# Kernel tuning notes

Hardware: AMD Instinct MI355X
Metric: run time of the kernel (lower is better)

The kernel has to match this reference:

```python
import jax, jax.numpy as jnp
import numpy as np

N, E, IN, H, D = 50000, 800000, 256, 4, 32
NEG_SLOPE = 0.2


def setup_inputs() -> dict:
    key = jax.random.key(0)
    ks = jax.random.split(key, 11)
    feat = jax.random.normal(ks[0], (N, IN), jnp.float32)
    src = jax.random.randint(ks[1], (E,), 0, N, jnp.int32)
    dst = jax.random.randint(ks[2], (E,), 0, N, jnp.int32)
    # ppmi in [1, 10) so log(log(ppmi)) path is non-trivial
    ppmi = 1.0 + 9.0 * jax.random.uniform(ks[3], (E,), jnp.float32)
    eps_src = jax.random.normal(ks[4], (N, H, 1), jnp.float32)
    eps_dst = jax.random.normal(ks[5], (N, H, 1), jnp.float32)
    W = jax.random.normal(ks[6], (IN, H * D), jnp.float32) * (1.0 / np.sqrt(IN))
    mu_src = jax.random.normal(ks[7], (1, H, D), jnp.float32) * 0.02
    mu_dst = jax.random.normal(ks[8], (1, H, D), jnp.float32) * 0.02
    lam_src = jax.random.normal(ks[9], (1, H, D), jnp.float32) * 0.02
    lam_dst = jax.random.normal(ks[10], (1, H, D), jnp.float32) * 0.02
    return dict(feat=feat, src=src, dst=dst, ppmi=ppmi, eps_src=eps_src,
                eps_dst=eps_dst, W=W, mu_src=mu_src, mu_dst=mu_dst,
                lam_src=lam_src, lam_dst=lam_dst)


def reference(feat, src, dst, ppmi, eps_src, eps_dst, W, mu_src, mu_dst, lam_src, lam_dst):
    n = feat.shape[0]
    h, d = mu_src.shape[1], mu_src.shape[2]
    ft = (feat @ W).reshape(n, h, d)                      # [N,H,D]
    # per-node attention scalars (src == dst node set here)
    mu_s = (ft * mu_src).sum(-1, keepdims=True)           # [N,H,1]
    lam_s = (ft * lam_src).sum(-1, keepdims=True)
    mu_d = (ft * mu_dst).sum(-1, keepdims=True)
    lam_d = (ft * lam_src).sum(-1, keepdims=True)         # original uses lam_src here (replicated)
    # reparameterize z = eps * exp(0.5*logvar) + mu
    z_src = eps_src * jnp.exp(0.5 * lam_s) + mu_s
    z_dst = eps_dst * jnp.exp(0.5 * lam_d) + mu_d
    e = jax.nn.leaky_relu(z_src[src] + z_dst[dst], NEG_SLOPE)   # [E,H,1]
    scale = jnp.clip(jnp.log(jnp.clip(jnp.log(ppmi), 1.0, None)), 1.0, None)
    e2 = e * scale[:, None, None]
    # edge softmax over destination segments
    emax = jax.ops.segment_max(e2, dst, num_segments=n)   # [N,H,1]
    ee = jnp.exp(e2 - emax[dst])
    denom = jax.ops.segment_sum(ee, dst, num_segments=n)
    a = ee / denom[dst]                                    # [E,H,1]
    # weighted scatter-sum aggregation: u_mul_e + sum
    rst = jax.ops.segment_sum(ft[src] * a, dst, num_segments=n)  # [N,H,D]
    return rst, mu_s + mu_d, lam_s + lam_d
```

## Files before the change

### kernel.cpp

```cpp
#include <hip/hip_runtime.h>

#define N_NODES 50000
#define N_EDGES 800000
#define IN_DIM  256
#define NH      4
#define HD      128
#define NEG_SLOPE 0.2f
#define SCAN_BLOCKS ((N_NODES + 255) / 256)

typedef short          v8s __attribute__((ext_vector_type(8)));
typedef float          v4f __attribute__((ext_vector_type(4)));
typedef unsigned short us8 __attribute__((ext_vector_type(8)));

__device__ __forceinline__ unsigned short f2bf(float f)
{
    unsigned int u = __float_as_uint(f);
    u += 0x7fffu + ((u >> 16) & 1u);
    return (unsigned short)(u >> 16);
}
__device__ __forceinline__ float bf2f(unsigned int bits16)
{
    return __uint_as_float(bits16 << 16);
}

__global__ __launch_bounds__(256) void k0_wt(
    const float* __restrict__ W, unsigned short* __restrict__ Wt_bf)
{
    const int idx = blockIdx.x * 256 + threadIdx.x;
    const int n = idx >> 8;
    const int k = idx & 255;
    Wt_bf[n * IN_DIM + k] = f2bf(W[(size_t)k * HD + n]);
}

#define AS 40
#define CS 136

__global__ __launch_bounds__(256) void k1_mfma(
    const float* __restrict__ feat, const unsigned short* __restrict__ Wt_bf,
    unsigned short* __restrict__ ft_bf)
{
    __shared__ ushort smem[17408];
    ushort* A_sh = smem;
    ushort* B_sh = smem + 128 * AS;

    const int t    = threadIdx.x;
    const int lane = t & 63;
    const int wv   = t >> 6;
    const int r0   = blockIdx.x * 128;

    const int arow = t >> 3;
    const int akk  = (t & 7) * 4;
    int rA[4];
#pragma unroll
    for (int p = 0; p < 4; ++p) rA[p] = min(r0 + arow + 32 * p, N_NODES - 1);
    const int bn  = t >> 2;
    const int bk8 = (t & 3) * 8;

    float4 fa[4];
    us8    fb[2];

#define LOADC(kc0)                                                              \
    do {                                                                        \
        _Pragma("unroll")                                                       \
        for (int p = 0; p < 4; ++p)                                             \
            fa[p] = *(const float4*)(feat + (size_t)rA[p] * IN_DIM + (kc0) + akk); \
        _Pragma("unroll")                                                       \
        for (int p = 0; p < 2; ++p)                                             \
            fb[p] = *(const us8*)(Wt_bf + (size_t)(bn + 64 * p) * IN_DIM + (kc0) + bk8); \
    } while (0)

    v4f acc[2][8];
#pragma unroll
    for (int i = 0; i < 2; ++i)
#pragma unroll
        for (int j = 0; j < 8; ++j) acc[i][j] = (v4f)(0.0f);

    const int frow = lane & 15;
    const int fq   = lane >> 4;

    LOADC(0);

    for (int c = 0; c < IN_DIM / 32; ++c) {
        __syncthreads();
#pragma unroll
        for (int p = 0; p < 4; ++p) {
            ushort4 u;
            u.x = f2bf(fa[p].x); u.y = f2bf(fa[p].y);
            u.z = f2bf(fa[p].z); u.w = f2bf(fa[p].w);
            *(ushort4*)(A_sh + (arow + 32 * p) * AS + akk) = u;
        }
#pragma unroll
        for (int p = 0; p < 2; ++p)
            *(us8*)(B_sh + (bn + 64 * p) * AS + bk8) = fb[p];
        __syncthreads();

        if (c + 1 < IN_DIM / 32) LOADC((c + 1) * 32);

        v8s a0 = *(const v8s*)(A_sh + (wv * 32 + frow) * AS + fq * 8);
        v8s a1 = *(const v8s*)(A_sh + (wv * 32 + 16 + frow) * AS + fq * 8);
        v8s bfr[8];
#pragma unroll
        for (int nf = 0; nf < 8; ++nf)
            bfr[nf] = *(const v8s*)(B_sh + (nf * 16 + frow) * AS + fq * 8);
#pragma unroll
        for (int nf = 0; nf < 8; ++nf) {
            acc[0][nf] = __builtin_amdgcn_mfma_f32_16x16x32_bf16(
                a0, bfr[nf], acc[0][nf], 0, 0, 0);
            acc[1][nf] = __builtin_amdgcn_mfma_f32_16x16x32_bf16(
                a1, bfr[nf], acc[1][nf], 0, 0, 0);
        }
    }

    __syncthreads();
    ushort* Cw = smem + wv * (32 * CS);
#pragma unroll
    for (int mf = 0; mf < 2; ++mf)
#pragma unroll
        for (int nf = 0; nf < 8; ++nf)
#pragma unroll
            for (int r = 0; r < 4; ++r)
                Cw[(mf * 16 + fq * 4 + r) * CS + nf * 16 + frow] =
                    f2bf(acc[mf][nf][r]);
    __syncthreads();

#pragma unroll
    for (int p = 0; p < 8; ++p) {
        const int row_l = (lane >> 4) + 4 * p;
        const int colv  = (lane & 15) * 8;
        const us8 val = *(const us8*)(Cw + row_l * CS + colv);
        const int grow = r0 + wv * 32 + row_l;
        if (grow < N_NODES)
            *(us8*)(ft_bf + (size_t)grow * HD + colv) = val;
    }
}

__global__ __launch_bounds__(256) void k1b_scalars(
    const unsigned short* __restrict__ ft_bf,
    const float* __restrict__ mu_src, const float* __restrict__ mu_dst,
    const float* __restrict__ lam_src,
    const float* __restrict__ eps_src, const float* __restrict__ eps_dst,
    float* __restrict__ z_src_ws, float* __restrict__ z_dst_ws,
    float* __restrict__ mu_out, float* __restrict__ lam_out)
{
    const int g = blockIdx.x * 256 + threadIdx.x;
    if (g >= N_NODES * NH) return;
    const int row = g >> 2;
    const int h   = g & 3;

    const unsigned short* fr = ft_bf + (size_t)row * HD + h * 32;
    const float* ms = mu_src + h * 32;
    const float* md = mu_dst + h * 32;
    const float* ls = lam_src + h * 32;

    float pm = 0.0f, pd = 0.0f, pl = 0.0f;
#pragma unroll
    for (int v = 0; v < 4; ++v) {
        const us8 u = *(const us8*)(fr + v * 8);
#pragma unroll
        for (int j = 0; j < 8; ++j) {
            const float f = bf2f(u[j]);
            const int   i = v * 8 + j;
            pm = fmaf(f, ms[i], pm);
            pd = fmaf(f, md[i], pd);
            pl = fmaf(f, ls[i], pl);
        }
    }
    const float sdev = expf(0.5f * pl);
    z_src_ws[g] = eps_src[g] * sdev + pm;
    z_dst_ws[g] = eps_dst[g] * sdev + pd;
    mu_out[g]   = pm + pd;
    lam_out[g]  = 2.0f * pl;
}

__device__ __forceinline__ void edge_w(float4 zs, float4 zd, float scale,
                                       float w[4])
{
    float z[4] = {zs.x + zd.x, zs.y + zd.y, zs.z + zd.z, zs.w + zd.w};
#pragma unroll
    for (int h = 0; h < 4; ++h) {
        float v = z[h];
        v = (v >= 0.0f) ? v : NEG_SLOPE * v;
        w[h] = __expf(v * scale);
    }
}

__device__ __forceinline__ float edge_scale(float p)
{
    const float lp = fmaxf(__logf(p), 1.0f);
    return fmaxf(__logf(lp), 1.0f);
}

__global__ __launch_bounds__(256) void k2_hist(
    const int* __restrict__ dst, int* __restrict__ counts)
{
    const int e = blockIdx.x * 256 + threadIdx.x;
    if (e < N_EDGES) atomicAdd(&counts[dst[e]], 1);
}

__global__ __launch_bounds__(256) void k_scan_local(
    const int* __restrict__ counts, int* __restrict__ local,
    int* __restrict__ bsums)
{
    __shared__ int sh[256];
    const int t = threadIdx.x;
    const int i = blockIdx.x * 256 + t;
    const int v = (i < N_NODES) ? counts[i] : 0;
    sh[t] = v;
    __syncthreads();
#pragma unroll
    for (int off = 1; off < 256; off <<= 1) {
        int x = (t >= off) ? sh[t - off] : 0;
        __syncthreads();
        sh[t] += x;
        __syncthreads();
    }
    if (i < N_NODES) local[i] = sh[t] - v;
    if (t == 255) bsums[blockIdx.x] = sh[255];
}

__global__ __launch_bounds__(256) void k_scan_bsums(
    const int* __restrict__ bsums, int* __restrict__ bscan)
{
    __shared__ int sh[256];
    const int t = threadIdx.x;
    const int v = (t < SCAN_BLOCKS) ? bsums[t] : 0;
    sh[t] = v;
    __syncthreads();
#pragma unroll
    for (int off = 1; off < 256; off <<= 1) {
        int x = (t >= off) ? sh[t - off] : 0;
        __syncthreads();
        sh[t] += x;
        __syncthreads();
    }
    if (t < SCAN_BLOCKS) bscan[t] = sh[t] - v;
}

__global__ __launch_bounds__(256) void k_scan_add(
    const int* __restrict__ local, const int* __restrict__ bscan,
    int* __restrict__ offsets, int* __restrict__ cursor)
{
    const int i = blockIdx.x * 256 + threadIdx.x;
    if (i >= N_NODES) return;
    const int o = local[i] + bscan[blockIdx.x];
    offsets[i] = o;
    cursor[i]  = o;
}

__global__ __launch_bounds__(256) void k_scatter(
    const int* __restrict__ src, const int* __restrict__ dst,
    const float* __restrict__ ppmi,
    const float4* __restrict__ z_src_ws, const float4* __restrict__ z_dst_ws,
    int* __restrict__ cursor, int4* __restrict__ rec_sorted)
{
    const int e = blockIdx.x * 256 + threadIdx.x;
    if (e >= N_EDGES) return;
    const int s  = src[e];
    const int d0 = dst[e];
    const int j  = atomicAdd(&cursor[d0], 1);

    float w[4];
    edge_w(z_src_ws[s], z_dst_ws[d0], edge_scale(ppmi[e]), w);
    int4 rec;
    rec.x = s;
    rec.y = (int)((unsigned)f2bf(w[0]) | ((unsigned)f2bf(w[1]) << 16));
    rec.z = (int)((unsigned)f2bf(w[2]) | ((unsigned)f2bf(w[3]) << 16));
    rec.w = 0;
    rec_sorted[j] = rec;
}

__global__ __launch_bounds__(64) void k3_csr(
    const int* __restrict__ offsets, const int* __restrict__ counts,
    const int4* __restrict__ rec_sorted,
    const unsigned int* __restrict__ ft_u32, float2* __restrict__ rst2)
{
    const int node = blockIdx.x;
    const int lane = threadIdx.x;
    const int h    = lane >> 4;
    const int start = offsets[node];
    const int end   = start + counts[node];

    float2 acc0 = make_float2(0.0f, 0.0f);
    float2 acc1 = make_float2(0.0f, 0.0f);
    float  wsum = 0.0f;

    int i = start;
    for (; i + 1 < end; i += 2) {
        const int4 r0 = rec_sorted[i];
        const int4 r1 = rec_sorted[i + 1];
        const unsigned f0 = ft_u32[(size_t)r0.x * (HD / 2) + lane];
        const unsigned f1 = ft_u32[(size_t)r1.x * (HD / 2) + lane];
        const unsigned p0 = (h < 2) ? (unsigned)r0.y : (unsigned)r0.z;
        const unsigned p1 = (h < 2) ? (unsigned)r1.y : (unsigned)r1.z;
        const float w0 = bf2f((h & 1) ? (p0 >> 16) : (p0 & 0xffffu));
        const float w1 = bf2f((h & 1) ? (p1 >> 16) : (p1 & 0xffffu));
        acc0.x = fmaf(bf2f(f0 & 0xffffu), w0, acc0.x);
        acc0.y = fmaf(bf2f(f0 >> 16),     w0, acc0.y);
        acc1.x = fmaf(bf2f(f1 & 0xffffu), w1, acc1.x);
        acc1.y = fmaf(bf2f(f1 >> 16),     w1, acc1.y);
        wsum += w0 + w1;
    }
    if (i < end) {
        const int4 r0 = rec_sorted[i];
        const unsigned f0 = ft_u32[(size_t)r0.x * (HD / 2) + lane];
        const unsigned p0 = (h < 2) ? (unsigned)r0.y : (unsigned)r0.z;
        const float w0 = bf2f((h & 1) ? (p0 >> 16) : (p0 & 0xffffu));
        acc0.x = fmaf(bf2f(f0 & 0xffffu), w0, acc0.x);
        acc0.y = fmaf(bf2f(f0 >> 16),     w0, acc0.y);
        wsum += w0;
    }
    acc0.x += acc1.x;
    acc0.y += acc1.y;
    const float inv = (wsum > 0.0f) ? 1.0f / wsum : 0.0f;
    rst2[(size_t)node * (HD / 2) + lane] =
        make_float2(acc0.x * inv, acc0.y * inv);
}

extern "C" void kernel_launch(void* const* d_in, const int* in_sizes, int n_in,
                              void* d_out, int out_size, void* d_ws, size_t ws_size,
                              hipStream_t stream)
{
    const float* feat    = (const float*)d_in[0];
    const int*   src     = (const int*)  d_in[1];
    const int*   dst     = (const int*)  d_in[2];
    const float* ppmi    = (const float*)d_in[3];
    const float* eps_src = (const float*)d_in[4];
    const float* eps_dst = (const float*)d_in[5];
    const float* W       = (const float*)d_in[6];
    const float* mu_src  = (const float*)d_in[7];
    const float* mu_dst  = (const float*)d_in[8];
    const float* lam_src = (const float*)d_in[9];

    float* out     = (float*)d_out;
    float* rst     = out;
    float* mu_out  = out + (size_t)N_NODES * HD;
    float* lam_out = mu_out + (size_t)N_NODES * NH;

    char* wsb = (char*)d_ws;
    int4*           rec_s  = (int4*)wsb;
    unsigned short* ft_bf  = (unsigned short*)(wsb + (size_t)N_EDGES * 16);
    unsigned short* Wt_bf  = ft_bf + (size_t)N_NODES * HD;
    float*          zs_ws  = (float*)(Wt_bf + (size_t)HD * IN_DIM);
    float*          zd_ws  = zs_ws + (size_t)N_NODES * NH;
    int*            counts = (int*)(zd_ws + (size_t)N_NODES * NH);
    int*            local  = counts + N_NODES;
    int*            offsets= local + N_NODES;
    int*            cursor = offsets + N_NODES;
    int*            bsums  = cursor + N_NODES;
    int*            bscan  = bsums + 256;

    hipMemsetAsync(counts, 0, N_NODES * sizeof(int), stream);

    k0_wt<<<(HD * IN_DIM) / 256, 256, 0, stream>>>(W, Wt_bf);

    k1_mfma<<<(N_NODES + 127) / 128, 256, 0, stream>>>(feat, Wt_bf, ft_bf);

    k1b_scalars<<<(N_NODES * NH + 255) / 256, 256, 0, stream>>>(
        ft_bf, mu_src, mu_dst, lam_src, eps_src, eps_dst,
        zs_ws, zd_ws, mu_out, lam_out);

    k2_hist<<<(N_EDGES + 255) / 256, 256, 0, stream>>>(dst, counts);

    k_scan_local<<<SCAN_BLOCKS, 256, 0, stream>>>(counts, local, bsums);
    k_scan_bsums<<<1, 256, 0, stream>>>(bsums, bscan);
    k_scan_add<<<SCAN_BLOCKS, 256, 0, stream>>>(local, bscan, offsets, cursor);

    k_scatter<<<(N_EDGES + 255) / 256, 256, 0, stream>>>(
        src, dst, ppmi, (const float4*)zs_ws, (const float4*)zd_ws,
        cursor, rec_s);

    k3_csr<<<N_NODES, 64, 0, stream>>>(
        offsets, counts, rec_s, (const unsigned int*)ft_bf, (float2*)rst);
}
```

Baseline: 262.2 us.

## Fuse independent launches and defer edge-weight computation into CSR aggregation

Merges the W transpose with the dst histogram, and the local scan with the per-node scalar kernel, into shared grids using block-index branching, removing two launches. The scatter now writes compact 8-byte records (src, edge scale) instead of 16-byte records with precomputed bf16 weights. The aggregation kernel recomputes the leaky-relu/exp weight per head from z_src/z_dst, with its edge loop unrolled by four. This cuts scatter traffic and weight quantisation but adds a gathered z_src load and an exp per lane per edge in the gather kernel.

```diff
diff --git a/kernel.cpp b/kernel.cpp
--- a/kernel.cpp
+++ b/kernel.cpp
@@ -7,6 +7,9 @@
 #define HD      128
 #define NEG_SLOPE 0.2f
 #define SCAN_BLOCKS ((N_NODES + 255) / 256)
+#define HIST_BLOCKS ((N_EDGES + 255) / 256)
+#define WT_BLOCKS   ((HD * IN_DIM) / 256)
+#define K1B_BLOCKS  ((N_NODES * NH + 255) / 256)
 
 typedef short          v8s __attribute__((ext_vector_type(8)));
 typedef float          v4f __attribute__((ext_vector_type(4)));
@@ -23,13 +26,26 @@
     return __uint_as_float(bits16 << 16);
 }
 
-__global__ __launch_bounds__(256) void k0_wt(
-    const float* __restrict__ W, unsigned short* __restrict__ Wt_bf)
-{
-    const int idx = blockIdx.x * 256 + threadIdx.x;
-    const int n = idx >> 8;
-    const int k = idx & 255;
-    Wt_bf[n * IN_DIM + k] = f2bf(W[(size_t)k * HD + n]);
+__device__ __forceinline__ float edge_scale(float p)
+{
+    const float lp = fmaxf(__logf(p), 1.0f);
+    return fmaxf(__logf(lp), 1.0f);
+}
+
+__global__ __launch_bounds__(256) void k_wt_hist(
+    const float* __restrict__ W, unsigned short* __restrict__ Wt_bf,
+    const int* __restrict__ dst, int* __restrict__ counts)
+{
+    const int b = blockIdx.x;
+    if (b < HIST_BLOCKS) {
+        const int e = b * 256 + threadIdx.x;
+        if (e < N_EDGES) atomicAdd(&counts[dst[e]], 1);
+    } else {
+        const int idx = (b - HIST_BLOCKS) * 256 + threadIdx.x;
+        const int n = idx >> 8;
+        const int k = idx & 255;
+        Wt_bf[n * IN_DIM + k] = f2bf(W[(size_t)k * HD + n]);
+    }
 }
 
 #define AS 40
@@ -134,7 +150,9 @@
     }
 }
 
-__global__ __launch_bounds__(256) void k1b_scalars(
+__global__ __launch_bounds__(256) void k_k1b_scanlocal(
+    const int* __restrict__ counts, int* __restrict__ local,
+    int* __restrict__ bsums,
     const unsigned short* __restrict__ ft_bf,
     const float* __restrict__ mu_src, const float* __restrict__ mu_dst,
     const float* __restrict__ lam_src,
@@ -142,7 +160,28 @@
     float* __restrict__ z_src_ws, float* __restrict__ z_dst_ws,
     float* __restrict__ mu_out, float* __restrict__ lam_out)
 {
-    const int g = blockIdx.x * 256 + threadIdx.x;
+    __shared__ int sh[256];
+    const int b = blockIdx.x;
+    const int t = threadIdx.x;
+
+    if (b < SCAN_BLOCKS) {
+        const int i = b * 256 + t;
+        const int v = (i < N_NODES) ? counts[i] : 0;
+        sh[t] = v;
+        __syncthreads();
+#pragma unroll
+        for (int off = 1; off < 256; off <<= 1) {
+            int x = (t >= off) ? sh[t - off] : 0;
+            __syncthreads();
+            sh[t] += x;
+            __syncthreads();
+        }
+        if (i < N_NODES) local[i] = sh[t] - v;
+        if (t == 255) bsums[b] = sh[255];
+        return;
+    }
+
+    const int g = (b - SCAN_BLOCKS) * 256 + t;
     if (g >= N_NODES * NH) return;
     const int row = g >> 2;
     const int h   = g & 3;
@@ -172,52 +211,6 @@
     lam_out[g]  = 2.0f * pl;
 }
 
-__device__ __forceinline__ void edge_w(float4 zs, float4 zd, float scale,
-                                       float w[4])
-{
-    float z[4] = {zs.x + zd.x, zs.y + zd.y, zs.z + zd.z, zs.w + zd.w};
-#pragma unroll
-    for (int h = 0; h < 4; ++h) {
-        float v = z[h];
-        v = (v >= 0.0f) ? v : NEG_SLOPE * v;
-        w[h] = __expf(v * scale);
-    }
-}
-
-__device__ __forceinline__ float edge_scale(float p)
-{
-    const float lp = fmaxf(__logf(p), 1.0f);
-    return fmaxf(__logf(lp), 1.0f);
-}
-
-__global__ __launch_bounds__(256) void k2_hist(
-    const int* __restrict__ dst, int* __restrict__ counts)
-{
-    const int e = blockIdx.x * 256 + threadIdx.x;
-    if (e < N_EDGES) atomicAdd(&counts[dst[e]], 1);
-}
-
-__global__ __launch_bounds__(256) void k_scan_local(
-    const int* __restrict__ counts, int* __restrict__ local,
-    int* __restrict__ bsums)
-{
-    __shared__ int sh[256];
-    const int t = threadIdx.x;
-    const int i = blockIdx.x * 256 + t;
-    const int v = (i < N_NODES) ? counts[i] : 0;
-    sh[t] = v;
-    __syncthreads();
-#pragma unroll
-    for (int off = 1; off < 256; off <<= 1) {
-        int x = (t >= off) ? sh[t - off] : 0;
-        __syncthreads();
-        sh[t] += x;
-        __syncthreads();
-    }
-    if (i < N_NODES) local[i] = sh[t] - v;
-    if (t == 255) bsums[blockIdx.x] = sh[255];
-}
-
 __global__ __launch_bounds__(256) void k_scan_bsums(
     const int* __restrict__ bsums, int* __restrict__ bscan)
 {
@@ -250,70 +243,78 @@
 __global__ __launch_bounds__(256) void k_scatter(
     const int* __restrict__ src, const int* __restrict__ dst,
     const float* __restrict__ ppmi,
-    const float4* __restrict__ z_src_ws, const float4* __restrict__ z_dst_ws,
-    int* __restrict__ cursor, int4* __restrict__ rec_sorted)
+    int* __restrict__ cursor, int2* __restrict__ rec_sorted)
 {
     const int e = blockIdx.x * 256 + threadIdx.x;
     if (e >= N_EDGES) return;
     const int s  = src[e];
     const int d0 = dst[e];
     const int j  = atomicAdd(&cursor[d0], 1);
-
-    float w[4];
-    edge_w(z_src_ws[s], z_dst_ws[d0], edge_scale(ppmi[e]), w);
-    int4 rec;
-    rec.x = s;
-    rec.y = (int)((unsigned)f2bf(w[0]) | ((unsigned)f2bf(w[1]) << 16));
-    rec.z = (int)((unsigned)f2bf(w[2]) | ((unsigned)f2bf(w[3]) << 16));
-    rec.w = 0;
-    rec_sorted[j] = rec;
+    rec_sorted[j] = make_int2(s, __float_as_int(edge_scale(ppmi[e])));
+}
+
+__device__ __forceinline__ float edge_w1(float zs, float zd, float sc)
+{
+    float v = zs + zd;
+    v = (v >= 0.0f) ? v : NEG_SLOPE * v;
+    return __expf(v * sc);
 }
 
 __global__ __launch_bounds__(64) void k3_csr(
     const int* __restrict__ offsets, const int* __restrict__ counts,
-    const int4* __restrict__ rec_sorted,
+    const int2* __restrict__ rec_sorted,
+    const float* __restrict__ z_src_ws, const float* __restrict__ z_dst_ws,
     const unsigned int* __restrict__ ft_u32, float2* __restrict__ rst2)
 {
     const int node = blockIdx.x;
     const int lane = threadIdx.x;
     const int h    = lane >> 4;
     const int start = offsets[node];
-    const int end   = start + counts[node];
-
-    float2 acc0 = make_float2(0.0f, 0.0f);
-    float2 acc1 = make_float2(0.0f, 0.0f);
-    float  wsum = 0.0f;
-
-    int i = start;
-    for (; i + 1 < end; i += 2) {
-        const int4 r0 = rec_sorted[i];
-        const int4 r1 = rec_sorted[i + 1];
+    const int deg   = counts[node];
+    const float zd  = z_dst_ws[node * NH + h];
+
+    float ax = 0.0f, ay = 0.0f, wsum = 0.0f;
+
+    int i = 0;
+    for (; i + 4 <= deg; i += 4) {
+        const int2 r0 = rec_sorted[start + i];
+        const int2 r1 = rec_sorted[start + i + 1];
+        const int2 r2 = rec_sorted[start + i + 2];
+        const int2 r3 = rec_sorted[start + i + 3];
+        const float z0 = z_src_ws[r0.x * NH + h];
+        const float z1 = z_src_ws[r1.x * NH + h];
+        const float z2 = z_src_ws[r2.x * NH + h];
+        const float z3 = z_src_ws[r3.x * NH + h];
         const unsigned f0 = ft_u32[(size_t)r0.x * (HD / 2) + lane];
         const unsigned f1 = ft_u32[(size_t)r1.x * (HD / 2) + lane];
-        const unsigned p0 = (h < 2) ? (unsigned)r0.y : (unsigned)r0.z;
-        const unsigned p1 = (h < 2) ? (unsigned)r1.y : (unsigned)r1.z;
-        const float w0 = bf2f((h & 1) ? (p0 >> 16) : (p0 & 0xffffu));
-        const float w1 = bf2f((h & 1) ? (p1 >> 16) : (p1 & 0xffffu));
-        acc0.x = fmaf(bf2f(f0 & 0xffffu), w0, acc0.x);
-        acc0.y = fmaf(bf2f(f0 >> 16),     w0, acc0.y);
-        acc1.x = fmaf(bf2f(f1 & 0xffffu), w1, acc1.x);
-        acc1.y = fmaf(bf2f(f1 >> 16),     w1, acc1.y);
-        wsum += w0 + w1;
-    }
-    if (i < end) {
-        const int4 r0 = rec_sorted[i];
+        const unsigned f2 = ft_u32[(size_t)r2.x * (HD / 2) + lane];
+        const unsigned f3 = ft_u32[(size_t)r3.x * (HD / 2) + lane];
+        const float w0 = edge_w1(z0, zd, __int_as_float(r0.y));
+        const float w1 = edge_w1(z1, zd, __int_as_float(r1.y));
+        const float w2 = edge_w1(z2, zd, __int_as_float(r2.y));
+        const float w3 = edge_w1(z3, zd, __int_as_float(r3.y));
+        ax = fmaf(bf2f(f0 & 0xffffu), w0, ax);
+        ay = fmaf(bf2f(f0 >> 16),     w0, ay);
+        ax = fmaf(bf2f(f1 & 0xffffu), w1, ax);
+        ay = fmaf(bf2f(f1 >> 16),     w1, ay);
+        ax = fmaf(bf2f(f2 & 0xffffu), w2, ax);
+        ay = fmaf(bf2f(f2 >> 16),     w2, ay);
+        ax = fmaf(bf2f(f3 & 0xffffu), w3, ax);
+        ay = fmaf(bf2f(f3 >> 16),     w3, ay);
+        wsum += (w0 + w1) + (w2 + w3);
+    }
+    for (; i < deg; ++i) {
+        const int2 r0 = rec_sorted[start + i];
+        const float z0 = z_src_ws[r0.x * NH + h];
         const unsigned f0 = ft_u32[(size_t)r0.x * (HD / 2) + lane];
-        const unsigned p0 = (h < 2) ? (unsigned)r0.y : (unsigned)r0.z;
-        const float w0 = bf2f((h & 1) ? (p0 >> 16) : (p0 & 0xffffu));
-        acc0.x = fmaf(bf2f(f0 & 0xffffu), w0, acc0.x);
-        acc0.y = fmaf(bf2f(f0 >> 16),     w0, acc0.y);
+        const float w0 = edge_w1(z0, zd, __int_as_float(r0.y));
+        ax = fmaf(bf2f(f0 & 0xffffu), w0, ax);
+        ay = fmaf(bf2f(f0 >> 16),     w0, ay);
         wsum += w0;
     }
-    acc0.x += acc1.x;
-    acc0.y += acc1.y;
+
     const float inv = (wsum > 0.0f) ? 1.0f / wsum : 0.0f;
-    rst2[(size_t)node * (HD / 2) + lane] =
-        make_float2(acc0.x * inv, acc0.y * inv);
+    rst2[(size_t)node * (HD / 2) + lane] = make_float2(ax * inv, ay * inv);
 }
 
 extern "C" void kernel_launch(void* const* d_in, const int* in_sizes, int n_in,
@@ -337,8 +338,8 @@
     float* lam_out = mu_out + (size_t)N_NODES * NH;
 
     char* wsb = (char*)d_ws;
-    int4*           rec_s  = (int4*)wsb;
-    unsigned short* ft_bf  = (unsigned short*)(wsb + (size_t)N_EDGES * 16);
+    int2*           rec_s  = (int2*)wsb;
+    unsigned short* ft_bf  = (unsigned short*)(wsb + (size_t)N_EDGES * 8);
     unsigned short* Wt_bf  = ft_bf + (size_t)N_NODES * HD;
     float*          zs_ws  = (float*)(Wt_bf + (size_t)HD * IN_DIM);
     float*          zd_ws  = zs_ws + (size_t)N_NODES * NH;
@@ -351,24 +352,22 @@
 
     hipMemsetAsync(counts, 0, N_NODES * sizeof(int), stream);
 
-    k0_wt<<<(HD * IN_DIM) / 256, 256, 0, stream>>>(W, Wt_bf);
+    k_wt_hist<<<HIST_BLOCKS + WT_BLOCKS, 256, 0, stream>>>(
+        W, Wt_bf, dst, counts);
 
     k1_mfma<<<(N_NODES + 127) / 128, 256, 0, stream>>>(feat, Wt_bf, ft_bf);
 
-    k1b_scalars<<<(N_NODES * NH + 255) / 256, 256, 0, stream>>>(
+    k_k1b_scanlocal<<<SCAN_BLOCKS + K1B_BLOCKS, 256, 0, stream>>>(
+        counts, local, bsums,
         ft_bf, mu_src, mu_dst, lam_src, eps_src, eps_dst,
         zs_ws, zd_ws, mu_out, lam_out);
 
-    k2_hist<<<(N_EDGES + 255) / 256, 256, 0, stream>>>(dst, counts);
-
-    k_scan_local<<<SCAN_BLOCKS, 256, 0, stream>>>(counts, local, bsums);
     k_scan_bsums<<<1, 256, 0, stream>>>(bsums, bscan);
     k_scan_add<<<SCAN_BLOCKS, 256, 0, stream>>>(local, bscan, offsets, cursor);
 
-    k_scatter<<<(N_EDGES + 255) / 256, 256, 0, stream>>>(
-        src, dst, ppmi, (const float4*)zs_ws, (const float4*)zd_ws,
-        cursor, rec_s);
+    k_scatter<<<HIST_BLOCKS, 256, 0, stream>>>(src, dst, ppmi, cursor, rec_s);
 
     k3_csr<<<N_NODES, 64, 0, stream>>>(
-        offsets, counts, rec_s, (const unsigned int*)ft_bf, (float2*)rst);
-}
+        offsets, counts, rec_s, zs_ws, zd_ws,
+        (const unsigned int*)ft_bf, (float2*)rst);
+}
```

After: 258.0 us. No clear change (-1.6%).
